# Performance work log

Hardware: AMD Instinct MI355X
Metric: run time of the kernel (lower is better)

Reference implementation:

```python
import jax, jax.numpy as jnp
import numpy as np

N, E, G = 100000, 500000, 1000


def _gat(h_in, src, dst, W, a_s, a_d, b, n):
    # PyG GATConv, heads=1, concat=True, negative_slope=0.2, self-loops already in src/dst
    h = h_in @ W.T                                  # [N, out]
    alpha_src = h @ a_s                             # [N]
    alpha_dst = h @ a_d                             # [N]
    e = jax.nn.leaky_relu(alpha_src[src] + alpha_dst[dst], 0.2)  # [E']
    m = jax.ops.segment_max(e, dst, num_segments=n)
    ex = jnp.exp(e - m[dst])
    den = jax.ops.segment_sum(ex, dst, num_segments=n)
    alpha = ex / den[dst]                           # segment softmax over incoming edges
    out = jax.ops.segment_sum(h[src] * alpha[:, None], dst, num_segments=n)
    return out + b


def _forward(x, edge_index, batch, w1, b1, w2, b2, w3, b3,
             g1w, g1as, g1ad, g1b, g2w, g2as, g2ad, g2b,
             g3w, g3as, g3ad, g3b, g4w, g4as, g4ad, g4b,
             g5w, g5as, g5ad, g5b, lw, lb):
    n = x.shape[0]
    h = jax.nn.relu(x @ w1.T + b1)
    h = jax.nn.relu(h @ w2.T + b2)
    h = jax.nn.relu(h @ w3.T + b3)
    loops = jnp.arange(n)
    src = jnp.concatenate([edge_index[0], loops])   # add self-loops
    dst = jnp.concatenate([edge_index[1], loops])
    h = jax.nn.relu(_gat(h, src, dst, g1w, g1as, g1ad, g1b, n))
    h = jax.nn.relu(_gat(h, src, dst, g2w, g2as, g2ad, g2b, n))
    h = jax.nn.relu(_gat(h, src, dst, g3w, g3as, g3ad, g3b, n))
    h = jax.nn.relu(_gat(h, src, dst, g4w, g4as, g4ad, g4b, n))
    h = jax.nn.relu(_gat(h, src, dst, g5w, g5as, g5ad, g5b, n))
    sums = jax.ops.segment_sum(h, batch, num_segments=G)            # [G,32]
    cnt = jax.ops.segment_sum(jnp.ones((n,), h.dtype), batch, num_segments=G)
    mean = sums / jnp.maximum(cnt, 1.0)[:, None]
    return jax.nn.sigmoid(mean @ lw.T + lb)         # [G,1]


def setup_inputs() -> dict:
    key = jax.random.key(0)
    ks = jax.random.split(key, 24)

    def lin(k, o, i):
        k1, k2 = jax.random.split(k)
        s = 1.0 / np.sqrt(i)
        return (jax.random.uniform(k1, (o, i), jnp.float32, -s, s),
                jax.random.uniform(k2, (o,), jnp.float32, -s, s))

    def gat_p(k, i, o):
        k1, k2, k3 = jax.random.split(k, 3)
        s = 1.0 / np.sqrt(i)
        W = jax.random.uniform(k1, (o, i), jnp.float32, -s, s)
        a_s = jax.random.normal(k2, (o,), jnp.float32) / np.sqrt(o)
        a_d = jax.random.normal(k3, (o,), jnp.float32) / np.sqrt(o)
        return W, a_s, a_d, jnp.zeros((o,), jnp.float32)

    inp = {}
    inp['x'] = jax.random.normal(ks[0], (N, 1), jnp.float32)
    inp['edge_index'] = jax.random.randint(ks[1], (2, E), 0, N)
    inp['batch'] = jnp.sort(jax.random.randint(ks[2], (N,), 0, G))
    inp['w1'], inp['b1'] = lin(ks[3], 16, 1)
    inp['w2'], inp['b2'] = lin(ks[4], 32, 16)
    inp['w3'], inp['b3'] = lin(ks[5], 64, 32)
    dims = [(64, 128), (128, 256), (256, 128), (128, 64), (64, 32)]
    for j, (i, o) in enumerate(dims, start=1):
        W, a_s, a_d, b = gat_p(ks[5 + j], i, o)
        inp[f'g{j}w'], inp[f'g{j}as'], inp[f'g{j}ad'], inp[f'g{j}b'] = W, a_s, a_d, b
    inp['lw'], inp['lb'] = lin(ks[12], 1, 32)
    return inp


def reference(x, edge_index, batch, w1, b1, w2, b2, w3, b3,
              g1w, g1as, g1ad, g1b, g2w, g2as, g2ad, g2b,
              g3w, g3as, g3ad, g3b, g4w, g4as, g4ad, g4b,
              g5w, g5as, g5ad, g5b, lw, lb):
    return _forward(x, edge_index, batch, w1, b1, w2, b2, w3, b3,
                    g1w, g1as, g1ad, g1b, g2w, g2as, g2ad, g2b,
                    g3w, g3as, g3ad, g3b, g4w, g4as, g4ad, g4b,
                    g5w, g5as, g5ad, g5b, lw, lb)
```

## Files before the change

kernel.cpp:

```cpp
#include <hip/hip_runtime.h>
#include <math.h>

typedef __attribute__((ext_vector_type(8))) __bf16 bf16x8;
typedef __attribute__((ext_vector_type(4))) float f32x4;

__device__ inline unsigned short f2bf(float f) {
    unsigned int i = __float_as_uint(f);
    unsigned int r = i + 0x7fffu + ((i >> 16) & 1u);
    return (unsigned short)(r >> 16);
}
__device__ inline float bf2f(unsigned short u) {
    return __uint_as_float(((unsigned int)u) << 16);
}

__global__ __launch_bounds__(256) void prelude_kernel(
    const float* __restrict__ x,
    const float* __restrict__ w1, const float* __restrict__ b1,
    const float* __restrict__ w2, const float* __restrict__ b2,
    const float* __restrict__ w3, const float* __restrict__ b3,
    unsigned short* __restrict__ h0, int n,
    const float* __restrict__ g0, const float* __restrict__ g1, const float* __restrict__ g2,
    const float* __restrict__ g3, const float* __restrict__ g4,
    unsigned short* __restrict__ wbAll,
    const int* __restrict__ batch, int* __restrict__ gstart, int G,
    const int* __restrict__ dst, int* __restrict__ deg, int E,
    int mlpB, int f2bfB, int gsB, int histB,
    const float* __restrict__ as1, const float* __restrict__ ad1,
    float* __restrict__ s1out, float* __restrict__ d1out,
    const float* __restrict__ as2, const float* __restrict__ ad2,
    float* __restrict__ pv2) {
    int b = blockIdx.x;
    int tid = threadIdx.x;
    if (b < mlpB) {
        __shared__ float4 psd1q[32];
        if (tid >= 192) {
            int i = tid - 192;
            float s = 0.f, d = 0.f;
            for (int o = 0; o < 128; o++) {
                float w = g0[o * 64 + i];
                s += as1[o] * w;
                d += ad1[o] * w;
            }
            ((float2*)psd1q)[i] = make_float2(s, d);
        }
        __syncthreads();
        int node = b * 256 + tid;
        if (node >= n) return;
        float xv = x[node];
        float t1[16], t2[32];
#pragma unroll
        for (int i = 0; i < 16; i++) t1[i] = fmaxf(w1[i] * xv + b1[i], 0.f);
        const float4* w2v = (const float4*)w2;
#pragma unroll
        for (int o = 0; o < 32; o++) {
            float a = b2[o];
#pragma unroll
            for (int q = 0; q < 4; q++) {
                float4 wv = w2v[o * 4 + q];
                a += wv.x * t1[q * 4] + wv.y * t1[q * 4 + 1] + wv.z * t1[q * 4 + 2] +
                     wv.w * t1[q * 4 + 3];
            }
            t2[o] = fmaxf(a, 0.f);
        }
        const float4* w3v = (const float4*)w3;
        float sdot = 0.f, ddot = 0.f;
        uint4* gp = (uint4*)(h0 + (size_t)node * 64);
#pragma unroll
        for (int c = 0; c < 8; c++) {
            unsigned int wvec[4];
#pragma unroll
            for (int p = 0; p < 4; p++) {
                int o = c * 8 + p * 2;
                float a0 = b3[o], a1 = b3[o + 1];
#pragma unroll
                for (int q = 0; q < 8; q++) {
                    float4 wa = w3v[o * 8 + q];
                    float4 wb = w3v[o * 8 + 8 + q];
                    a0 += wa.x * t2[q * 4] + wa.y * t2[q * 4 + 1] + wa.z * t2[q * 4 + 2] +
                          wa.w * t2[q * 4 + 3];
                    a1 += wb.x * t2[q * 4] + wb.y * t2[q * 4 + 1] + wb.z * t2[q * 4 + 2] +
                          wb.w * t2[q * 4 + 3];
                }
                float r0 = fmaxf(a0, 0.f), r1 = fmaxf(a1, 0.f);
                float4 qsd = psd1q[o >> 1];
                sdot += r0 * qsd.x + r1 * qsd.z;
                ddot += r0 * qsd.y + r1 * qsd.w;
                wvec[p] = (unsigned)f2bf(r0) | ((unsigned)f2bf(r1) << 16);
            }
            gp[c] = make_uint4(wvec[0], wvec[1], wvec[2], wvec[3]);
        }
        s1out[node] = sdot;
        d1out[node] = ddot;
    } else if (b < mlpB + f2bfB) {
        int i = (b - mlpB) * 256 + tid;
        float v;
        if (i < 8192) v = g0[i];
        else if (i < 40960) v = g1[i - 8192];
        else if (i < 73728) v = g2[i - 40960];
        else if (i < 81920) v = g3[i - 73728];
        else if (i < 83968) v = g4[i - 81920];
        else return;
        wbAll[i] = f2bf(v);
    } else if (b < mlpB + f2bfB + gsB) {
        int g = (b - mlpB - f2bfB) * 256 + tid;
        if (g > G) return;
        if (g == G) { gstart[G] = n; return; }
        int lo = 0, hi = n;
        while (lo < hi) {
            int mid = (lo + hi) >> 1;
            if (batch[mid] < g) lo = mid + 1;
            else hi = mid;
        }
        gstart[g] = lo;
    } else if (b < mlpB + f2bfB + gsB + histB) {
        int e = (b - mlpB - f2bfB - gsB) * 256 + tid;
        if (e >= E + n) return;
        int d = (e < E) ? dst[e] : (e - E);
        atomicAdd(&deg[d], 1);
    } else {
        if (tid < 128) {
            float s = 0.f;
            for (int o = 0; o < 256; o++) s += as2[o] * g1[o * 128 + tid];
            pv2[tid] = s;
        } else {
            int c = tid - 128;
            float s = 0.f;
            for (int o = 0; o < 256; o++) s += ad2[o] * g1[o * 128 + c];
            pv2[128 + c] = s;
        }
    }
}

template <int BN, int EPI>
__global__ __launch_bounds__(256) void gemm_mfma(
    const unsigned short* __restrict__ A, const unsigned short* __restrict__ Wb,
    unsigned short* __restrict__ Cb,
    const float* __restrict__ avs, const float* __restrict__ avd,
    float* __restrict__ as_, float* __restrict__ ad_,
    const float* __restrict__ bias, int n, int K, int O) {
    constexpr int SN = BN / 32;
    __shared__ unsigned short As[128][72];
    __shared__ unsigned short Ws[BN][72];
    int tid = threadIdx.x;
    int row0 = blockIdx.x * 128, col0 = blockIdx.y * BN;
    int w = tid >> 6, lane = tid & 63;
    int wr = w >> 1, wc = w & 1;
    int quad = lane >> 4, l15 = lane & 15;
    f32x4 acc[4][SN];
#pragma unroll
    for (int mi = 0; mi < 4; mi++)
#pragma unroll
        for (int ni = 0; ni < SN; ni++) acc[mi][ni] = (f32x4){0.f, 0.f, 0.f, 0.f};

    for (int k0 = 0; k0 < K; k0 += 64) {
#pragma unroll
        for (int i = tid; i < 1024; i += 256) {
            int r = i >> 3, c8 = i & 7;
            int gr = row0 + r;
            uint4 v = make_uint4(0u, 0u, 0u, 0u);
            if (gr < n) v = *(const uint4*)(A + (size_t)gr * K + k0 + c8 * 8);
            *(uint4*)&As[r][c8 * 8] = v;
        }
#pragma unroll
        for (int i = tid; i < BN * 8; i += 256) {
            int r = i >> 3, c8 = i & 7;
            uint4 v = *(const uint4*)(Wb + (size_t)(col0 + r) * K + k0 + c8 * 8);
            *(uint4*)&Ws[r][c8 * 8] = v;
        }
        __syncthreads();
#pragma unroll
        for (int kk = 0; kk < 64; kk += 32) {
            bf16x8 bfr[SN];
#pragma unroll
            for (int ni = 0; ni < SN; ni++)
                bfr[ni] = *(const bf16x8*)&Ws[wc * (BN / 2) + ni * 16 + l15][kk + quad * 8];
#pragma unroll
            for (int mi = 0; mi < 4; mi++) {
                bf16x8 afr = *(const bf16x8*)&As[wr * 64 + mi * 16 + l15][kk + quad * 8];
#pragma unroll
                for (int ni = 0; ni < SN; ni++)
                    acc[mi][ni] = __builtin_amdgcn_mfma_f32_16x16x32_bf16(afr, bfr[ni],
                                                                          acc[mi][ni], 0, 0, 0);
            }
        }
        __syncthreads();
    }
    float avsv[SN], avdv[SN], bv[SN];
    int gc[SN];
#pragma unroll
    for (int ni = 0; ni < SN; ni++) {
        gc[ni] = col0 + wc * (BN / 2) + ni * 16 + l15;
        if constexpr (EPI != 2) {
            avsv[ni] = avs[gc[ni]];
            avdv[ni] = avd[gc[ni]];
        }
        if constexpr (EPI >= 1) bv[ni] = bias[gc[ni]];
    }
#pragma unroll
    for (int mi = 0; mi < 4; mi++) {
        int gm0 = row0 + wr * 64 + mi * 16 + quad * 4;
        float ps[4] = {0.f, 0.f, 0.f, 0.f}, pd[4] = {0.f, 0.f, 0.f, 0.f};
#pragma unroll
        for (int ni = 0; ni < SN; ni++) {
#pragma unroll
            for (int r = 0; r < 4; r++) {
                float d = acc[mi][ni][r];
                if constexpr (EPI >= 1) d = fmaxf(d + bv[ni], 0.f);
                int gm = gm0 + r;
                if (gm < n) Cb[(size_t)gm * O + gc[ni]] = f2bf(d);
                if constexpr (EPI != 2) {
                    ps[r] += d * avsv[ni];
                    pd[r] += d * avdv[ni];
                }
            }
        }
        if constexpr (EPI != 2) {
#pragma unroll
            for (int r = 0; r < 4; r++) {
#pragma unroll
                for (int m = 1; m <= 8; m <<= 1) {
                    ps[r] += __shfl_xor(ps[r], m);
                    pd[r] += __shfl_xor(pd[r], m);
                }
            }
            if (l15 == 0) {
#pragma unroll
                for (int r = 0; r < 4; r++) {
                    int gm = gm0 + r;
                    if (gm < n) {
                        atomicAdd(&as_[gm], ps[r]);
                        atomicAdd(&ad_[gm], pd[r]);
                    }
                }
            }
        }
    }
}

__global__ void scan_block_sums(const int* __restrict__ deg, int* __restrict__ bsums, int n) {
    __shared__ int sdata[256];
    int tid = threadIdx.x;
    int base = blockIdx.x * 1024 + tid * 4;
    int s = 0;
    for (int i = 0; i < 4; i++) {
        int g = base + i;
        if (g < n) s += deg[g];
    }
    sdata[tid] = s;
    __syncthreads();
    for (int off = 128; off > 0; off >>= 1) {
        if (tid < off) sdata[tid] += sdata[tid + off];
        __syncthreads();
    }
    if (tid == 0) bsums[blockIdx.x] = sdata[0];
}

__global__ void scan_write(const int* __restrict__ deg, const int* __restrict__ bsums,
                           int* __restrict__ rowptr, int* __restrict__ cursor, int n, int nb) {
    __shared__ int sdata[256];
    int tid = threadIdx.x;
    sdata[tid] = (tid < blockIdx.x && tid < nb) ? bsums[tid] : 0;
    __syncthreads();
    for (int off = 128; off > 0; off >>= 1) {
        if (tid < off) sdata[tid] += sdata[tid + off];
        __syncthreads();
    }
    int base = sdata[0];
    __syncthreads();
    int gbase = blockIdx.x * 1024 + tid * 4;
    int v[4];
    int s = 0;
    for (int i = 0; i < 4; i++) {
        int g = gbase + i;
        v[i] = (g < n) ? deg[g] : 0;
        s += v[i];
    }
    sdata[tid] = s;
    __syncthreads();
    for (int off = 1; off < 256; off <<= 1) {
        int t = (tid >= off) ? sdata[tid - off] : 0;
        __syncthreads();
        sdata[tid] += t;
        __syncthreads();
    }
    int excl = sdata[tid] - s + base;
    for (int i = 0; i < 4; i++) {
        int g = gbase + i;
        if (g < n) { rowptr[g] = excl; cursor[g] = excl; }
        excl += v[i];
    }
    if (blockIdx.x == gridDim.x - 1 && tid == 255) rowptr[n] = base + sdata[255];
}

__global__ void scatter_kernel(const int* __restrict__ esrc_in, const int* __restrict__ edst_in,
                               int* __restrict__ cursor, int* __restrict__ esrc, int E, int n) {
    int e = blockIdx.x * 256 + threadIdx.x;
    if (e >= E + n) return;
    int s, d;
    if (e < E) { s = esrc_in[e]; d = edst_in[e]; }
    else { s = e - E; d = e - E; }
    int pos = atomicAdd(&cursor[d], 1);
    esrc[pos] = s;
}

template <int O, bool BIASRELU>
__global__ __launch_bounds__(256) void gat_aggregate(
    const unsigned short* __restrict__ hl, const float* __restrict__ as_,
    const float* __restrict__ ad_, const int* __restrict__ rowptr,
    const int* __restrict__ esrc, const float* __restrict__ bias,
    unsigned short* __restrict__ hout, int n, float* __restrict__ zeroBuf, int zeroCnt) {
    int gtid = blockIdx.x * 256 + threadIdx.x;
    if (gtid < zeroCnt) zeroBuf[gtid] = 0.f;
    constexpr int C8 = O / 8;
    constexpr int EPP = 16 / C8;
    int tid = threadIdx.x;
    int v = blockIdx.x * 16 + (tid >> 4);
    int l = tid & 15;
    int gbase = tid & 48;
    if (v >= n) return;
    int beg = rowptr[v], end = rowptr[v + 1];
    int deg = end - beg;
    float adv = ad_[v];
    int sub = l / C8;
    int c = l % C8;
    float acc[8] = {0.f, 0.f, 0.f, 0.f, 0.f, 0.f, 0.f, 0.f};
    if (deg <= 16) {
        int sreg = v;
        float e = -1e30f;
        if (l < deg) {
            sreg = esrc[beg + l];
            float t = as_[sreg] + adv;
            e = (t > 0.f) ? t : 0.2f * t;
        }
        float m = e;
#pragma unroll
        for (int o = 8; o > 0; o >>= 1) m = fmaxf(m, __shfl_xor(m, o));
        float ex = (l < deg) ? __expf(e - m) : 0.f;
        float sum = ex;
#pragma unroll
        for (int o = 8; o > 0; o >>= 1) sum += __shfl_xor(sum, o);
        float alpha_r = ex / sum;
        for (int j0 = 0; j0 < deg; j0 += EPP) {
            int idx = j0 + sub;
            int cidx = (idx < deg) ? idx : 0;
            float alpha = __shfl(alpha_r, gbase + cidx);
            int s2 = __shfl(sreg, gbase + cidx);
            if (idx >= deg) alpha = 0.f;
            uint4 raw = ((const uint4*)(hl + (size_t)s2 * O))[c];
            acc[0] += alpha * __uint_as_float(raw.x << 16);
            acc[1] += alpha * __uint_as_float(raw.x & 0xffff0000u);
            acc[2] += alpha * __uint_as_float(raw.y << 16);
            acc[3] += alpha * __uint_as_float(raw.y & 0xffff0000u);
            acc[4] += alpha * __uint_as_float(raw.z << 16);
            acc[5] += alpha * __uint_as_float(raw.z & 0xffff0000u);
            acc[6] += alpha * __uint_as_float(raw.w << 16);
            acc[7] += alpha * __uint_as_float(raw.w & 0xffff0000u);
        }
    } else {
        float mymax = -1e30f;
        for (int j = beg + l; j < end; j += 16) {
            float e = as_[esrc[j]] + adv;
            e = (e > 0.f) ? e : 0.2f * e;
            mymax = fmaxf(mymax, e);
        }
#pragma unroll
        for (int o = 8; o > 0; o >>= 1) mymax = fmaxf(mymax, __shfl_xor(mymax, o));
        float mysum = 0.f;
        for (int j = beg + l; j < end; j += 16) {
            float e = as_[esrc[j]] + adv;
            e = (e > 0.f) ? e : 0.2f * e;
            mysum += __expf(e - mymax);
        }
#pragma unroll
        for (int o = 8; o > 0; o >>= 1) mysum += __shfl_xor(mysum, o);
        float invden = 1.f / mysum;
        for (int j0 = beg; j0 < end; j0 += EPP) {
            int j = j0 + sub;
            bool valid = j < end;
            int s = valid ? esrc[j] : v;
            float e = as_[s] + adv;
            e = (e > 0.f) ? e : 0.2f * e;
            float alpha = valid ? __expf(e - mymax) * invden : 0.f;
            uint4 raw = ((const uint4*)(hl + (size_t)s * O))[c];
            acc[0] += alpha * __uint_as_float(raw.x << 16);
            acc[1] += alpha * __uint_as_float(raw.x & 0xffff0000u);
            acc[2] += alpha * __uint_as_float(raw.y << 16);
            acc[3] += alpha * __uint_as_float(raw.y & 0xffff0000u);
            acc[4] += alpha * __uint_as_float(raw.z << 16);
            acc[5] += alpha * __uint_as_float(raw.z & 0xffff0000u);
            acc[6] += alpha * __uint_as_float(raw.w << 16);
            acc[7] += alpha * __uint_as_float(raw.w & 0xffff0000u);
        }
    }
#pragma unroll
    for (int o = C8; o < 16; o <<= 1)
#pragma unroll
        for (int k = 0; k < 8; k++) acc[k] += __shfl_xor(acc[k], o);
    if (l < C8) {
        unsigned short ov[8];
#pragma unroll
        for (int k = 0; k < 8; k++) {
            float val = acc[k];
            if constexpr (BIASRELU) val = fmaxf(val + bias[c * 8 + k], 0.f);
            ov[k] = f2bf(val);
        }
        uint4 packed;
        packed.x = (unsigned)ov[0] | ((unsigned)ov[1] << 16);
        packed.y = (unsigned)ov[2] | ((unsigned)ov[3] << 16);
        packed.z = (unsigned)ov[4] | ((unsigned)ov[5] << 16);
        packed.w = (unsigned)ov[6] | ((unsigned)ov[7] << 16);
        ((uint4*)(hout + (size_t)v * O))[c] = packed;
    }
}

__global__ __launch_bounds__(256) void pool_final_kernel(
    const unsigned short* __restrict__ h, const int* __restrict__ start,
    const float* __restrict__ lw, const float* __restrict__ lb,
    float* __restrict__ out, int G) {
    __shared__ float red[8][33];
    int g = blockIdx.x;
    if (g >= G) return;
    int beg = start[g], end = start[g + 1];
    int tid = threadIdx.x;
    int nodeLane = tid >> 5, f = tid & 31;
    float acc = 0.f;
    for (int v = beg + nodeLane; v < end; v += 8)
        acc += bf2f(h[(size_t)v * 32 + f]);
    red[nodeLane][f] = acc;
    __syncthreads();
    if (tid < 32) {
        float s = 0.f;
#pragma unroll
        for (int i = 0; i < 8; i++) s += red[i][f];
        float inv = 1.f / fmaxf((float)(end - beg), 1.f);
        float val = s * inv * lw[f];
#pragma unroll
        for (int o = 16; o > 0; o >>= 1) val += __shfl_xor(val, o);
        if (f == 0) out[g] = 1.f / (1.f + __expf(-(val + lb[0])));
    }
}

extern "C" void kernel_launch(void* const* d_in, const int* in_sizes, int n_in,
                              void* d_out, int out_size, void* d_ws, size_t ws_size,
                              hipStream_t stream) {
    const float* x = (const float*)d_in[0];
    const int* ei = (const int*)d_in[1];
    const int* batch = (const int*)d_in[2];
    const float* w1 = (const float*)d_in[3];
    const float* b1 = (const float*)d_in[4];
    const float* w2 = (const float*)d_in[5];
    const float* b2 = (const float*)d_in[6];
    const float* w3 = (const float*)d_in[7];
    const float* b3 = (const float*)d_in[8];
    const float* gw[5];
    const float* gas[5];
    const float* gad[5];
    const float* gb[5];
    for (int l = 0; l < 5; l++) {
        gw[l] = (const float*)d_in[9 + l * 4 + 0];
        gas[l] = (const float*)d_in[9 + l * 4 + 1];
        gad[l] = (const float*)d_in[9 + l * 4 + 2];
        gb[l] = (const float*)d_in[9 + l * 4 + 3];
    }
    const float* lw = (const float*)d_in[29];
    const float* lb = (const float*)d_in[30];
    float* out = (float*)d_out;

    int N = in_sizes[0];
    int E = in_sizes[1] / 2;
    int G = out_size;
    int Etot = E + N;

    char* ws = (char*)d_ws;
    size_t off = 0;
    auto alloc = [&](size_t bytes) -> void* {
        void* p = ws + off;
        off = (off + bytes + 255) & ~(size_t)255;
        return p;
    };
    unsigned short* actA = (unsigned short*)alloc((size_t)N * 256 * 2);
    unsigned short* actB = (unsigned short*)alloc((size_t)N * 256 * 2);
    char* zblock = (char*)alloc((size_t)N * 20);
    float* sd2 = (float*)zblock;
    float* sd3 = sd2 + (size_t)N * 2;
    int* deg = (int*)(zblock + (size_t)N * 16);
    float* sd1 = (float*)alloc((size_t)N * 2 * 4);
    float* pv2 = (float*)alloc(256 * 4);
    int* rowptr = (int*)alloc((size_t)(N + 1) * 4);
    int* cursor = (int*)alloc((size_t)(N + 1) * 4);
    int* esrc = (int*)alloc((size_t)Etot * 4);
    int* bsums = (int*)alloc(4096);
    int* gstart = (int*)alloc((size_t)(G + 1) * 4);
    unsigned short* wbAll = (unsigned short*)alloc((size_t)83968 * 2);
    const int woff[5] = {0, 8192, 40960, 73728, 81920};
    unsigned short* wb[5];
    for (int l = 0; l < 5; l++) wb[l] = wbAll + woff[l];
    (void)ws_size;
    (void)n_in;

    hipMemsetAsync(zblock, 0, (size_t)N * 20, stream);

    int mlpB = (N + 255) / 256;
    int f2bfB = (83968 + 255) / 256;
    int gsB = (G + 1 + 255) / 256;
    int histB = (Etot + 255) / 256;
    prelude_kernel<<<mlpB + f2bfB + gsB + histB + 1, 256, 0, stream>>>(
        x, w1, b1, w2, b2, w3, b3, actA, N, gw[0], gw[1], gw[2], gw[3], gw[4], wbAll, batch,
        gstart, G, ei + E, deg, E, mlpB, f2bfB, gsB, histB,
        gas[0], gad[0], sd1, sd1 + N, gas[1], gad[1], pv2);

    int nb = (N + 1023) / 1024;
    scan_block_sums<<<nb, 256, 0, stream>>>(deg, bsums, N);
    scan_write<<<nb, 256, 0, stream>>>(deg, bsums, rowptr, cursor, N, nb);
    scatter_kernel<<<(Etot + 255) / 256, 256, 0, stream>>>(ei, ei + E, cursor, esrc, E, N);

    int aggBlocks = (N + 15) / 16;
    int gx = (N + 127) / 128;

    gat_aggregate<64, false><<<aggBlocks, 256, 0, stream>>>(
        actA, sd1, sd1 + N, rowptr, esrc, nullptr, actB, N, nullptr, 0);
    {
        dim3 grid(gx, 1);
        gemm_mfma<128, 1><<<grid, 256, 0, stream>>>(actB, wb[0], actA, pv2, pv2 + 128, sd2,
                                                    sd2 + N, gb[0], N, 64, 128);
    }

    gat_aggregate<128, false><<<aggBlocks, 256, 0, stream>>>(
        actA, sd2, sd2 + N, rowptr, esrc, nullptr, actB, N, sd1, 2 * N);
    {
        dim3 grid(gx, 2);
        gemm_mfma<128, 2><<<grid, 256, 0, stream>>>(actB, wb[1], actA, nullptr, nullptr,
                                                    nullptr, nullptr, gb[1], N, 128, 256);
    }

    {
        dim3 grid(gx, 1);
        gemm_mfma<128, 0><<<grid, 256, 0, stream>>>(actA, wb[2], actB, gas[2], gad[2], sd3,
                                                    sd3 + N, nullptr, N, 256, 128);
    }
    gat_aggregate<128, true><<<aggBlocks, 256, 0, stream>>>(
        actB, sd3, sd3 + N, rowptr, esrc, gb[2], actA, N, sd2, 2 * N);

    {
        dim3 grid(gx, 1);
        gemm_mfma<64, 0><<<grid, 256, 0, stream>>>(actA, wb[3], actB, gas[3], gad[3], sd1,
                                                   sd1 + N, nullptr, N, 128, 64);
    }
    gat_aggregate<64, true><<<aggBlocks, 256, 0, stream>>>(
        actB, sd1, sd1 + N, rowptr, esrc, gb[3], actA, N, nullptr, 0);

    {
        dim3 grid(gx, 1);
        gemm_mfma<32, 0><<<grid, 256, 0, stream>>>(actA, wb[4], actB, gas[4], gad[4], sd2,
                                                   sd2 + N, nullptr, N, 64, 32);
    }
    gat_aggregate<32, true><<<aggBlocks, 256, 0, stream>>>(
        actB, sd2, sd2 + N, rowptr, esrc, gb[4], actA, N, nullptr, 0);

    pool_final_kernel<<<G, 256, 0, stream>>>(actA, gstart, lw, lb, out, G);
}
```

Baseline: 482.8 us.

## Split prelude MLP across four threads per node and narrow GEMM column tiles

```diff
diff --git a/kernel.cpp b/kernel.cpp
--- a/kernel.cpp
+++ b/kernel.cpp
@@ -32,7 +32,16 @@
     int b = blockIdx.x;
     int tid = threadIdx.x;
     if (b < mlpB) {
+        __shared__ float sw1[16], sb1[16], sb2[32], sb3[64];
+        __shared__ float4 sw2q[128];
+        __shared__ float4 sw3q[576];
         __shared__ float4 psd1q[32];
+        if (tid < 16) { sw1[tid] = w1[tid]; sb1[tid] = b1[tid]; }
+        if (tid < 32) sb2[tid] = b2[tid];
+        if (tid < 64) sb3[tid] = b3[tid];
+        for (int i = tid; i < 128; i += 256) sw2q[i] = ((const float4*)w2)[i];
+        for (int i = tid; i < 512; i += 256)
+            sw3q[(i >> 3) * 9 + (i & 7)] = ((const float4*)w3)[i];
         if (tid >= 192) {
             int i = tid - 192;
             float s = 0.f, d = 0.f;
@@ -44,53 +53,53 @@
             ((float2*)psd1q)[i] = make_float2(s, d);
         }
         __syncthreads();
-        int node = b * 256 + tid;
+        int node = b * 64 + (tid >> 2);
+        int sub = tid & 3;
         if (node >= n) return;
         float xv = x[node];
         float t1[16], t2[32];
 #pragma unroll
-        for (int i = 0; i < 16; i++) t1[i] = fmaxf(w1[i] * xv + b1[i], 0.f);
-        const float4* w2v = (const float4*)w2;
+        for (int i = 0; i < 16; i++) t1[i] = fmaxf(sw1[i] * xv + sb1[i], 0.f);
 #pragma unroll
         for (int o = 0; o < 32; o++) {
-            float a = b2[o];
+            float a = sb2[o];
 #pragma unroll
             for (int q = 0; q < 4; q++) {
-                float4 wv = w2v[o * 4 + q];
+                float4 wv = sw2q[o * 4 + q];
                 a += wv.x * t1[q * 4] + wv.y * t1[q * 4 + 1] + wv.z * t1[q * 4 + 2] +
                      wv.w * t1[q * 4 + 3];
             }
             t2[o] = fmaxf(a, 0.f);
         }
-        const float4* w3v = (const float4*)w3;
         float sdot = 0.f, ddot = 0.f;
-        uint4* gp = (uint4*)(h0 + (size_t)node * 64);
-#pragma unroll
-        for (int c = 0; c < 8; c++) {
-            unsigned int wvec[4];
-#pragma unroll
-            for (int p = 0; p < 4; p++) {
-                int o = c * 8 + p * 2;
-                float a0 = b3[o], a1 = b3[o + 1];
-#pragma unroll
-                for (int q = 0; q < 8; q++) {
-                    float4 wa = w3v[o * 8 + q];
-                    float4 wb = w3v[o * 8 + 8 + q];
-                    a0 += wa.x * t2[q * 4] + wa.y * t2[q * 4 + 1] + wa.z * t2[q * 4 + 2] +
-                          wa.w * t2[q * 4 + 3];
-                    a1 += wb.x * t2[q * 4] + wb.y * t2[q * 4 + 1] + wb.z * t2[q * 4 + 2] +
-                          wb.w * t2[q * 4 + 3];
-                }
-                float r0 = fmaxf(a0, 0.f), r1 = fmaxf(a1, 0.f);
-                float4 qsd = psd1q[o >> 1];
-                sdot += r0 * qsd.x + r1 * qsd.z;
-                ddot += r0 * qsd.y + r1 * qsd.w;
-                wvec[p] = (unsigned)f2bf(r0) | ((unsigned)f2bf(r1) << 16);
-            }
-            gp[c] = make_uint4(wvec[0], wvec[1], wvec[2], wvec[3]);
-        }
-        s1out[node] = sdot;
-        d1out[node] = ddot;
+        unsigned int* gpw = (unsigned int*)(h0 + (size_t)node * 64);
+#pragma unroll
+        for (int p = 0; p < 8; p++) {
+            int o = p * 8 + sub * 2;
+            float a0 = sb3[o], a1 = sb3[o + 1];
+#pragma unroll
+            for (int q = 0; q < 8; q++) {
+                float4 wa = sw3q[o * 9 + q];
+                float4 wb = sw3q[(o + 1) * 9 + q];
+                a0 += wa.x * t2[q * 4] + wa.y * t2[q * 4 + 1] + wa.z * t2[q * 4 + 2] +
+                      wa.w * t2[q * 4 + 3];
+                a1 += wb.x * t2[q * 4] + wb.y * t2[q * 4 + 1] + wb.z * t2[q * 4 + 2] +
+                      wb.w * t2[q * 4 + 3];
+            }
+            float r0 = fmaxf(a0, 0.f), r1 = fmaxf(a1, 0.f);
+            float4 qsd = psd1q[o >> 1];
+            sdot += r0 * qsd.x + r1 * qsd.z;
+            ddot += r0 * qsd.y + r1 * qsd.w;
+            gpw[p * 4 + sub] = (unsigned)f2bf(r0) | ((unsigned)f2bf(r1) << 16);
+        }
+        sdot += __shfl_xor(sdot, 1);
+        sdot += __shfl_xor(sdot, 2);
+        ddot += __shfl_xor(ddot, 1);
+        ddot += __shfl_xor(ddot, 2);
+        if (sub == 0) {
+            s1out[node] = sdot;
+            d1out[node] = ddot;
+        }
     } else if (b < mlpB + f2bfB) {
         int i = (b - mlpB) * 256 + tid;
         float v;
@@ -500,7 +509,7 @@
 
     hipMemsetAsync(zblock, 0, (size_t)N * 20, stream);
 
-    int mlpB = (N + 255) / 256;
+    int mlpB = (N + 63) / 64;
     int f2bfB = (83968 + 255) / 256;
     int gsB = (G + 1 + 255) / 256;
     int histB = (Etot + 255) / 256;
@@ -520,23 +529,23 @@
     gat_aggregate<64, false><<<aggBlocks, 256, 0, stream>>>(
         actA, sd1, sd1 + N, rowptr, esrc, nullptr, actB, N, nullptr, 0);
     {
-        dim3 grid(gx, 1);
-        gemm_mfma<128, 1><<<grid, 256, 0, stream>>>(actB, wb[0], actA, pv2, pv2 + 128, sd2,
-                                                    sd2 + N, gb[0], N, 64, 128);
+        dim3 grid(gx, 2);
+        gemm_mfma<64, 1><<<grid, 256, 0, stream>>>(actB, wb[0], actA, pv2, pv2 + 128, sd2,
+                                                   sd2 + N, gb[0], N, 64, 128);
     }
 
     gat_aggregate<128, false><<<aggBlocks, 256, 0, stream>>>(
         actA, sd2, sd2 + N, rowptr, esrc, nullptr, actB, N, sd1, 2 * N);
     {
+        dim3 grid(gx, 4);
+        gemm_mfma<64, 2><<<grid, 256, 0, stream>>>(actB, wb[1], actA, nullptr, nullptr,
+                                                   nullptr, nullptr, gb[1], N, 128, 256);
+    }
+
+    {
         dim3 grid(gx, 2);
-        gemm_mfma<128, 2><<<grid, 256, 0, stream>>>(actB, wb[1], actA, nullptr, nullptr,
-                                                    nullptr, nullptr, gb[1], N, 128, 256);
-    }
-
-    {
-        dim3 grid(gx, 1);
-        gemm_mfma<128, 0><<<grid, 256, 0, stream>>>(actA, wb[2], actB, gas[2], gad[2], sd3,
-                                                    sd3 + N, nullptr, N, 256, 128);
+        gemm_mfma<64, 0><<<grid, 256, 0, stream>>>(actA, wb[2], actB, gas[2], gad[2], sd3,
+                                                   sd3 + N, nullptr, N, 256, 128);
     }
     gat_aggregate<128, true><<<aggBlocks, 256, 0, stream>>>(
         actB, sd3, sd3 + N, rowptr, esrc, gb[2], actA, N, sd2, 2 * N);
```

After: 459.2 us. 1.05x faster.
